# Optimization experiments

Hardware: AMD Instinct MI355X
Metric: run time of the kernel (lower is better)

The kernel has to match this reference:

```python
import jax, jax.numpy as jnp
import numpy as np

B, D, F = 4096, 2048, 16384


def setup_inputs() -> dict:
    key = jax.random.key(0)
    ks = jax.random.split(key, 5)
    s_enc = 1.0 / np.sqrt(D)
    s_dec = 1.0 / np.sqrt(F)
    return {
        "x": jax.random.normal(ks[0], (B, D), dtype=jnp.float32),
        "W_enc": jax.random.normal(ks[1], (F, D), dtype=jnp.float32) * s_enc,
        "b_enc": jnp.zeros((F,), dtype=jnp.float32),
        "W_kest1": jax.random.normal(ks[2], (F, D), dtype=jnp.float32) * s_enc,
        "b_kest1": jnp.zeros((F,), dtype=jnp.float32),
        "W_kest2": jax.random.normal(ks[3], (1, F), dtype=jnp.float32) * s_dec,
        "b_kest2": jnp.zeros((1,), dtype=jnp.float32),
        "W_dec": jax.random.normal(ks[4], (D, F), dtype=jnp.float32) * s_dec,
        "b_dec": jnp.zeros((D,), dtype=jnp.float32),
        "k": 64,
    }


def topk_per_row(acts, k_est):
    # rank of each element when sorted descending (ties resolved stably;
    # after ReLU ties are zeros, so output is identical either way)
    order = jnp.argsort(-acts, axis=1)          # [B, F] descending order
    rank = jnp.argsort(order, axis=1)           # rank[i,j] = position of acts[i,j]
    mask = rank < k_est[:, None]                # per-row dynamic (float) k
    return acts * mask


def reference(x, W_enc, b_enc, W_kest1, b_kest1, W_kest2, b_kest2, W_dec, b_dec, k):
    xc = x - b_dec                                              # [B, D]
    acts = jax.nn.relu(xc @ W_enc.T + b_enc)                    # [B, F]
    h = jax.nn.relu(xc @ W_kest1.T + b_kest1)                   # [B, F]
    k_est = jax.nn.sigmoid(h @ W_kest2.T + b_kest2)[:, 0] * (2.0 * k)  # [B]
    enc = topk_per_row(acts, k_est)                             # [B, F] sparse codes
    x_hat = enc @ W_dec.T + b_dec                               # [B, D]
    return x_hat
```

## Files before the change

kernel.cpp:

```cpp
#include <hip/hip_runtime.h>
#include <hip/hip_bf16.h>
#include <cstdint>
#include <cstddef>

#define BATCH 4096
#define DIM   2048
#define FEAT  16384
#define MAXF  2048

typedef __attribute__((ext_vector_type(8))) short s8v;
typedef __attribute__((ext_vector_type(8))) _Float16 h8v;
typedef __attribute__((ext_vector_type(4))) float f4v;

__device__ __forceinline__ void split2(float v, unsigned short &h, unsigned short &l){
  _Float16 hf = (_Float16)v;
  _Float16 lf = (_Float16)((v - (float)hf) * 2048.0f);
  h = __builtin_bit_cast(unsigned short, hf);
  l = __builtin_bit_cast(unsigned short, lf);
}

__device__ __forceinline__ void gload16(const void* g, void* l){
  __builtin_amdgcn_global_load_lds(
      (const __attribute__((address_space(1))) void*)g,
      (__attribute__((address_space(3))) void*)l, 16, 0, 0);
}

__global__ __launch_bounds__(256)
void splitX(const float* __restrict__ x, const float* __restrict__ bdec,
            unsigned short* __restrict__ p0, unsigned short* __restrict__ p1)
{
  const size_t i = ((size_t)blockIdx.x * 256 + threadIdx.x) * 4;
  const int col = (int)(i & (DIM - 1));
  const float4 v = *(const float4*)(x + i);
  const float4 b = *(const float4*)(bdec + col);
  float e0 = v.x - b.x, e1 = v.y - b.y, e2 = v.z - b.z, e3 = v.w - b.w;
  ushort4 H, L;
  split2(e0, H.x, L.x); split2(e1, H.y, L.y);
  split2(e2, H.z, L.z); split2(e3, H.w, L.w);
  *(ushort4*)(p0 + i) = H; *(ushort4*)(p1 + i) = L;
}

__global__ __launch_bounds__(256)
void splitW(const float* __restrict__ w,
            unsigned short* __restrict__ p0, unsigned short* __restrict__ p1)
{
  const size_t i = ((size_t)blockIdx.x * 256 + threadIdx.x) * 4;
  const float4 v = *(const float4*)(w + i);
  ushort4 H, L;
  split2(v.x, H.x, L.x); split2(v.y, H.y, L.y);
  split2(v.z, H.z, L.z); split2(v.w, H.w, L.w);
  *(ushort4*)(p0 + i) = H; *(ushort4*)(p1 + i) = L;
}

__global__ __launch_bounds__(256)
void splitW1(const float* __restrict__ w, unsigned short* __restrict__ p0)
{
  const size_t i = ((size_t)blockIdx.x * 256 + threadIdx.x) * 4;
  const float4 v = *(const float4*)(w + i);
  ushort4 H;
  H.x = __builtin_bit_cast(unsigned short, (_Float16)v.x);
  H.y = __builtin_bit_cast(unsigned short, (_Float16)v.y);
  H.z = __builtin_bit_cast(unsigned short, (_Float16)v.z);
  H.w = __builtin_bit_cast(unsigned short, (_Float16)v.w);
  *(ushort4*)(p0 + i) = H;
}

template<int MODE>
__global__ __launch_bounds__(256, 4)
void gemma(const unsigned short* __restrict__ Ah_, const unsigned short* __restrict__ Bh_,
           const float* __restrict__ bias, const float* __restrict__ w2,
           float* __restrict__ acts, float* __restrict__ zpart)
{
  __shared__ unsigned short sAB[2][2][128][32];
  const int tid  = threadIdx.x;
  const int lane = tid & 63, wv = tid >> 6;

  const int bid = blockIdx.x;
  const int xcd = bid & 7;
  const int idx = bid >> 3;
  const int sq  = idx >> 6;
  const int s   = idx & 63;
  const int bx  = (xcd << 4) | ((sq & 1) << 3) | (s & 7);
  const int by  = ((sq >> 1) << 3) | (s >> 3);
  const int row0 = by << 7, col0 = bx << 7;

  const int wr = (wv & 1) << 6, wc = (wv >> 1) << 6;

  f4v acc[4][4];
  #pragma unroll
  for (int i = 0; i < 4; ++i)
    #pragma unroll
    for (int j = 0; j < 4; ++j)
      acc[i][j] = (f4v){0.f, 0.f, 0.f, 0.f};

  const unsigned short* gsrc[4];
  unsigned ldsoff[4];
  #pragma unroll
  for (int j = 0; j < 4; ++j){
    const int q = (wv << 2) + j;
    const int mat = q >> 3;
    const int chunk = q & 7;
    const int r  = (chunk << 4) + (lane >> 2);
    const int gl = (lane & 3) ^ ((r >> 1) & 3);
    const int rowg = ((mat == 0) ? row0 : col0) + r;
    gsrc[j]  = ((mat == 0) ? Ah_ : Bh_) + (size_t)rowg * DIM + (gl << 3);
    ldsoff[j] = (unsigned)(mat * 8192 + chunk * 1024);
  }

  const int fr16 = lane & 15;
  const int kg   = lane >> 4;
  int ra[4], rb[4];
  #pragma unroll
  for (int f = 0; f < 4; ++f){ ra[f] = wr + (f << 4) + fr16; rb[f] = wc + (f << 4) + fr16; }

  #define LDFRAGA(bf, mat, r) \
    (*(const h8v*)((const char*)sAB + (bf) * 16384 + (mat) * 8192 + (r) * 64 + (((kg ^ (((r) >> 1) & 3)) << 4))))
  #define STAGEA(bf, ko)                                                      \
    {                                                                         \
      _Pragma("unroll")                                                       \
      for (int j = 0; j < 4; ++j)                                             \
        gload16(gsrc[j] + (ko), (char*)sAB + (bf) * 16384 + ldsoff[j]);       \
    }

  int cur = 0;
  STAGEA(0, 0);
  __syncthreads();

  for (int kt = 0; kt < DIM / 32; ++kt){
    if (kt < DIM / 32 - 1) STAGEA(cur ^ 1, (kt + 1) << 5);

    h8v Ahf[4], Bhf[4];
    #pragma unroll
    for (int f = 0; f < 4; ++f) Ahf[f] = LDFRAGA(cur, 0, ra[f]);
    #pragma unroll
    for (int f = 0; f < 4; ++f) Bhf[f] = LDFRAGA(cur, 1, rb[f]);
    #pragma unroll
    for (int fi = 0; fi < 4; ++fi)
      #pragma unroll
      for (int fj = 0; fj < 4; ++fj)
        acc[fi][fj] = __builtin_amdgcn_mfma_f32_16x16x32_f16(Bhf[fj], Ahf[fi], acc[fi][fj], 0, 0, 0);

    __syncthreads();
    cur ^= 1;
  }
  #undef LDFRAGA
  #undef STAGEA

  const int mloc = lane & 15;
  const int nq   = (lane >> 4) << 2;
  if (MODE == 0){
    #pragma unroll
    for (int fi = 0; fi < 4; ++fi){
      const int grow = row0 + wr + (fi << 4) + mloc;
      #pragma unroll
      for (int fj = 0; fj < 4; ++fj){
        const int gcol = col0 + wc + (fj << 4) + nq;
        const float4 be = *(const float4*)(bias + gcol);
        f4v v;
        v[0] = fmaxf(acc[fi][fj][0] + be.x, 0.f);
        v[1] = fmaxf(acc[fi][fj][1] + be.y, 0.f);
        v[2] = fmaxf(acc[fi][fj][2] + be.z, 0.f);
        v[3] = fmaxf(acc[fi][fj][3] + be.w, 0.f);
        __builtin_nontemporal_store(v, (f4v*)(acts + (size_t)grow * FEAT + gcol));
      }
    }
  } else {
    #pragma unroll
    for (int fi = 0; fi < 4; ++fi){
      float ssum = 0.f;
      #pragma unroll
      for (int fj = 0; fj < 4; ++fj){
        const int gcol = col0 + wc + (fj << 4) + nq;
        const float4 be = *(const float4*)(bias + gcol);
        const float4 wk = *(const float4*)(w2 + gcol);
        float h0 = fmaxf(acc[fi][fj][0] + be.x, 0.f);
        float h1 = fmaxf(acc[fi][fj][1] + be.y, 0.f);
        float h2 = fmaxf(acc[fi][fj][2] + be.z, 0.f);
        float h3 = fmaxf(acc[fi][fj][3] + be.w, 0.f);
        ssum = fmaf(h0, wk.x, ssum);
        ssum = fmaf(h1, wk.y, ssum);
        ssum = fmaf(h2, wk.z, ssum);
        ssum = fmaf(h3, wk.w, ssum);
      }
      ssum += __shfl_xor(ssum, 16);
      ssum += __shfl_xor(ssum, 32);
      if (lane < 16){
        const int grow = row0 + wr + (fi << 4) + lane;
        zpart[(size_t)grow * 256 + (bx << 1) + (wc >> 6)] = ssum;
      }
    }
  }
}

__global__ __launch_bounds__(512, 4)
void gemmx(const unsigned short* __restrict__ Ah_, const unsigned short* __restrict__ Al_,
           const unsigned short* __restrict__ Bh_, const unsigned short* __restrict__ Bl_,
           const float* __restrict__ bias, const float* __restrict__ w2,
           const int* __restrict__ rowList, const int* __restrict__ nflagp,
           float* __restrict__ zexact)
{
  const int panel = blockIdx.x >> 7;
  const int bx    = blockIdx.x & 127;
  const int row0p = panel << 7;
  if (row0p >= *nflagp) return;
  const int col0 = bx << 7;

  __shared__ unsigned short sAB[2][2][128][64];
  const int tid  = threadIdx.x;
  const int lane = tid & 63, wv = tid >> 6;
  const int wr = (wv & 3) << 5, wc = (wv >> 2) << 6;

  f4v acc[2][4], acc2[2][4];
  #pragma unroll
  for (int i = 0; i < 2; ++i)
    #pragma unroll
    for (int j = 0; j < 4; ++j){
      acc[i][j]  = (f4v){0.f, 0.f, 0.f, 0.f};
      acc2[i][j] = (f4v){0.f, 0.f, 0.f, 0.f};
    }

  const unsigned short* gsrc[4];
  unsigned ldsoff[4];
  #pragma unroll
  for (int j = 0; j < 4; ++j){
    const int q = (wv << 2) + j;
    const int mat = q >> 4;
    const int chunk = q & 15;
    const int r  = (chunk << 3) + (lane >> 3);
    const int gl = (lane & 7) ^ (r & 7);
    const int co = (gl & 3) << 3;
    const unsigned short* hi = (mat == 0) ? Ah_ : Bh_;
    const unsigned short* lo = (mat == 0) ? Al_ : Bl_;
    const int rowg = (mat == 0) ? rowList[row0p + r] : (col0 + r);
    gsrc[j]  = ((gl < 4) ? hi : lo) + (size_t)rowg * DIM + co;
    ldsoff[j] = (unsigned)(mat * 16384 + chunk * 1024);
  }

  const int fr16 = lane & 15;
  const int kg   = lane >> 4;
  int ra[2], rb[4];
  #pragma unroll
  for (int f = 0; f < 2; ++f) ra[f] = wr + (f << 4) + fr16;
  #pragma unroll
  for (int f = 0; f < 4; ++f) rb[f] = wc + (f << 4) + fr16;

  #define LDFRAG(bf, mat, r, hb) \
    (*(const h8v*)((const char*)sAB + (bf) * 32768 + (mat) * 16384 + (r) * 128 + (((((hb) + kg) ^ ((r) & 7)) << 4))))
  #define STAGE(bf, ko)                                                       \
    {                                                                         \
      _Pragma("unroll")                                                       \
      for (int j = 0; j < 4; ++j)                                             \
        gload16(gsrc[j] + (ko), (char*)sAB + (bf) * 32768 + ldsoff[j]);       \
    }

  int cur = 0;
  STAGE(0, 0);
  __syncthreads();

  for (int kt = 0; kt < DIM / 32; ++kt){
    if (kt < DIM / 32 - 1) STAGE(cur ^ 1, (kt + 1) << 5);

    h8v Ahf[2], Bhf[4], Xl[4];
    #pragma unroll
    for (int f = 0; f < 2; ++f) Ahf[f] = LDFRAG(cur, 0, ra[f], 0);
    #pragma unroll
    for (int f = 0; f < 4; ++f) Bhf[f] = LDFRAG(cur, 1, rb[f], 0);
    #pragma unroll
    for (int fi = 0; fi < 2; ++fi)
      #pragma unroll
      for (int fj = 0; fj < 4; ++fj)
        acc[fi][fj] = __builtin_amdgcn_mfma_f32_16x16x32_f16(Bhf[fj], Ahf[fi], acc[fi][fj], 0, 0, 0);
    #pragma unroll
    for (int f = 0; f < 2; ++f) Xl[f] = LDFRAG(cur, 0, ra[f], 4);
    #pragma unroll
    for (int fi = 0; fi < 2; ++fi)
      #pragma unroll
      for (int fj = 0; fj < 4; ++fj)
        acc2[fi][fj] = __builtin_amdgcn_mfma_f32_16x16x32_f16(Bhf[fj], Xl[fi], acc2[fi][fj], 0, 0, 0);
    #pragma unroll
    for (int f = 0; f < 4; ++f) Xl[f] = LDFRAG(cur, 1, rb[f], 4);
    #pragma unroll
    for (int fi = 0; fi < 2; ++fi)
      #pragma unroll
      for (int fj = 0; fj < 4; ++fj)
        acc2[fi][fj] = __builtin_amdgcn_mfma_f32_16x16x32_f16(Xl[fj], Ahf[fi], acc2[fi][fj], 0, 0, 0);

    __syncthreads();
    cur ^= 1;
  }
  #undef LDFRAG
  #undef STAGE

  const float LSC = 1.0f / 2048.0f;
  const int nq = (lane >> 4) << 2;
  #pragma unroll
  for (int fi = 0; fi < 2; ++fi){
    float ssum = 0.f;
    #pragma unroll
    for (int fj = 0; fj < 4; ++fj){
      const int gcol = col0 + wc + (fj << 4) + nq;
      const float4 be = *(const float4*)(bias + gcol);
      const float4 wk = *(const float4*)(w2 + gcol);
      float h0 = fmaxf(acc[fi][fj][0] + LSC * acc2[fi][fj][0] + be.x, 0.f);
      float h1 = fmaxf(acc[fi][fj][1] + LSC * acc2[fi][fj][1] + be.y, 0.f);
      float h2 = fmaxf(acc[fi][fj][2] + LSC * acc2[fi][fj][2] + be.z, 0.f);
      float h3 = fmaxf(acc[fi][fj][3] + LSC * acc2[fi][fj][3] + be.w, 0.f);
      ssum = fmaf(h0, wk.x, ssum);
      ssum = fmaf(h1, wk.y, ssum);
      ssum = fmaf(h2, wk.z, ssum);
      ssum = fmaf(h3, wk.w, ssum);
    }
    ssum += __shfl_xor(ssum, 16);
    ssum += __shfl_xor(ssum, 32);
    if (lane < 16){
      const int pos = row0p + wr + (fi << 4) + lane;
      zexact[(size_t)pos * 256 + (bx << 1) + (wc >> 6)] = ssum;
    }
  }
}

__global__ __launch_bounds__(256)
void zinit(int* __restrict__ rowList, int* __restrict__ nflag)
{
  const int i = blockIdx.x * 256 + threadIdx.x;
  if (i < MAXF) rowList[i] = 0;
  if (i == 0) *nflag = 0;
}

__global__ __launch_bounds__(256)
void zreduce_flag(const float* __restrict__ zpart, const float* __restrict__ bk2,
                  const int* __restrict__ kp, int* __restrict__ mrow,
                  int* __restrict__ rowList, int* __restrict__ nflag)
{
  const int row  = blockIdx.x * 4 + (threadIdx.x >> 6);
  const int lane = threadIdx.x & 63;
  const float* zp = zpart + (size_t)row * 256;
  float s = zp[lane] + zp[lane + 64] + zp[lane + 128] + zp[lane + 192];
  s += __shfl_xor(s, 1);
  s += __shfl_xor(s, 2);
  s += __shfl_xor(s, 4);
  s += __shfl_xor(s, 8);
  s += __shfl_xor(s, 16);
  s += __shfl_xor(s, 32);
  if (lane == 0){
    float z = s + bk2[0];
    float kest = 2.f * (float)(*kp) * (1.f / (1.f + expf(-z)));
    int m = (int)ceilf(kest);
    m = min(max(m, 0), 128);
    mrow[row] = m;
    const float frac = kest - floorf(kest);
    const float dmin = fminf(frac, 1.f - frac);
    if (dmin < 0.1f){
      int p = atomicAdd(nflag, 1);
      if (p < MAXF) rowList[p] = row;
    }
  }
}

__global__ __launch_bounds__(256)
void zreduce2(const float* __restrict__ zexact, const int* __restrict__ rowList,
              const int* __restrict__ nflagp, const float* __restrict__ bk2,
              const int* __restrict__ kp, int* __restrict__ mrow)
{
  const int pos  = blockIdx.x * 4 + (threadIdx.x >> 6);
  const int lane = threadIdx.x & 63;
  const int nf = min(*nflagp, MAXF);
  if (pos >= nf) return;
  const float* zp = zexact + (size_t)pos * 256;
  float s = zp[lane] + zp[lane + 64] + zp[lane + 128] + zp[lane + 192];
  s += __shfl_xor(s, 1);
  s += __shfl_xor(s, 2);
  s += __shfl_xor(s, 4);
  s += __shfl_xor(s, 8);
  s += __shfl_xor(s, 16);
  s += __shfl_xor(s, 32);
  if (lane == 0){
    float z = s + bk2[0];
    float kest = 2.f * (float)(*kp) * (1.f / (1.f + expf(-z)));
    int m = (int)ceilf(kest);
    m = min(max(m, 0), 128);
    mrow[rowList[pos]] = m;
  }
}

__device__ __forceinline__ void radix_find(int* hist, int nbins, int need, int tid,
                                           int* out3, int* blksum)
{
  const int per  = nbins >> 8;
  const int base = tid * per;
  int bs = 0;
  for (int j = 0; j < per; ++j) bs += hist[base + j];
  blksum[tid] = bs;
  __syncthreads();
  if (tid == 0){
    int a2 = 0;
    for (int t = 255; t >= 0; --t){ int v = blksum[t]; blksum[t] = a2; a2 += v; }
  }
  __syncthreads();
  int ch = blksum[tid];
  for (int j = per - 1; j >= 0; --j){
    const int b = base + j;
    const int c = hist[b];
    if (ch < need && need <= ch + c){ out3[0] = b; out3[1] = need - ch; out3[2] = ch; }
    ch += c;
  }
  __syncthreads();
}

__global__ __launch_bounds__(256)
void select_band(const float* __restrict__ acts, const float* __restrict__ x,
                 const float* __restrict__ bdec, const float* __restrict__ Wenc,
                 const int* __restrict__ mrow, int* __restrict__ selIdx,
                 float* __restrict__ selVal, int* __restrict__ scount)
{
  __shared__ int hist[2048];
  __shared__ int blksum[256];
  __shared__ int out3[4];
  __shared__ unsigned listU[2048];
  __shared__ int listI[2048];
  __shared__ int lcnt, dcnt, acnt;
  __shared__ unsigned ambU[64];
  __shared__ int ambI[64];
  __shared__ double ambE[64];
  __shared__ double wred[4];

  const int row = blockIdx.x, tid = threadIdx.x;
  const int m = mrow[row];
  const float* rp = acts + (size_t)row * FEAT;
  const int base = row << 7;

  for (int i = tid; i < 2048; i += 256) hist[i] = 0;
  __syncthreads();
  for (int it = 0; it < 16; ++it){
    const int i4 = (it << 8) + tid;
    const uint4 u4 = *(const uint4*)(rp + ((size_t)i4 << 2));
    if (u4.x) atomicAdd(&hist[u4.x >> 21], 1);
    if (u4.y) atomicAdd(&hist[u4.y >> 21], 1);
    if (u4.z) atomicAdd(&hist[u4.z >> 21], 1);
    if (u4.w) atomicAdd(&hist[u4.w >> 21], 1);
  }
  __syncthreads();
  radix_find(hist, 2048, m, tid, out3, blksum);
  const int bin1 = out3[0];
  const int rem1 = out3[1];
  const int bin1m1 = (bin1 > 1) ? bin1 - 1 : 1;

  if (tid == 0){ lcnt = 0; dcnt = 0; acnt = 0; }
  __syncthreads();
  for (int it = 0; it < 16; ++it){
    const int i4 = (it << 8) + tid;
    const uint4 u4 = *(const uint4*)(rp + ((size_t)i4 << 2));
    const int ib = i4 << 2;
    if (u4.x && (int)(u4.x >> 21) >= bin1m1){ int p = atomicAdd(&lcnt, 1); if (p < 2048){ listU[p] = u4.x; listI[p] = ib;     } }
    if (u4.y && (int)(u4.y >> 21) >= bin1m1){ int p = atomicAdd(&lcnt, 1); if (p < 2048){ listU[p] = u4.y; listI[p] = ib + 1; } }
    if (u4.z && (int)(u4.z >> 21) >= bin1m1){ int p = atomicAdd(&lcnt, 1); if (p < 2048){ listU[p] = u4.z; listI[p] = ib + 2; } }
    if (u4.w && (int)(u4.w >> 21) >= bin1m1){ int p = atomicAdd(&lcnt, 1); if (p < 2048){ listU[p] = u4.w; listI[p] = ib + 3; } }
  }
  __syncthreads();
  const int L = min(lcnt, 2048);

  for (int i = tid; i < 2048; i += 256) hist[i] = 0;
  __syncthreads();
  for (int i = tid; i < L; i += 256){
    unsigned u = listU[i];
    if ((int)(u >> 21) == bin1) atomicAdd(&hist[(u >> 10) & 0x7FF], 1);
  }
  __syncthreads();
  radix_find(hist, 2048, rem1, tid, out3, blksum);
  const int bin2 = out3[0];
  const int rem2 = out3[1];

  const unsigned topbits = (((unsigned)bin1 << 11) | (unsigned)bin2);
  for (int i = tid; i < 1024; i += 256) hist[i] = 0;
  __syncthreads();
  for (int i = tid; i < L; i += 256){
    unsigned u = listU[i];
    if ((u >> 10) == topbits) atomicAdd(&hist[u & 0x3FF], 1);
  }
  __syncthreads();
  radix_find(hist, 1024, rem2, tid, out3, blksum);
  const int bin3 = out3[0];

  const unsigned tbits = ((unsigned)bin1 << 21) | ((unsigned)bin2 << 10) | (unsigned)bin3;
  const float vm = __uint_as_float(tbits);
  const float EPS2 = 0.01f;
  const float lo_cut = vm - EPS2, hi_cut = vm + EPS2;

  for (int i = tid; i < L; i += 256){
    const float f = __uint_as_float(listU[i]);
    if (f > hi_cut){
      int p = atomicAdd(&dcnt, 1);
      selIdx[base + p] = listI[i];
      selVal[base + p] = f;
    } else if (f >= lo_cut){
      int p = atomicAdd(&acnt, 1);
      if (p < 64){ ambU[p] = listU[i]; ambI[p] = listI[i]; }
    }
  }
  __syncthreads();
  const int D = dcnt;
  const int A = min(acnt, 64);
  int need = m - D;
  if (need < 0) need = 0;
  if (need > A) need = A;

  if (need > 0){
    float* xcs = (float*)hist;
    for (int j = tid; j < DIM; j += 256)
      xcs[j] = x[(size_t)row * DIM + j] - bdec[j];
    __syncthreads();
    const int lane = tid & 63, wv = tid >> 6;
    for (int c = 0; c < A; ++c){
      const float* wrow = Wenc + (size_t)ambI[c] * DIM;
      double sd = 0.0;
      for (int j = tid; j < DIM; j += 256)
        sd += (double)xcs[j] * (double)wrow[j];
      #pragma unroll
      for (int off = 32; off; off >>= 1) sd += __shfl_xor(sd, off);
      if (lane == 0) wred[wv] = sd;
      __syncthreads();
      if (tid == 0) ambE[c] = wred[0] + wred[1] + wred[2] + wred[3];
      __syncthreads();
    }
    if (tid == 0){
      for (int e = 0; e < need; ++e){
        int best = -1;
        for (int c = 0; c < A; ++c){
          if (ambI[c] < 0) continue;
          if (best < 0 || ambE[c] > ambE[best] ||
              (ambE[c] == ambE[best] && ambI[c] < ambI[best])) best = c;
        }
        selIdx[base + D + e] = ambI[best];
        selVal[base + D + e] = __uint_as_float(ambU[best]);
        ambI[best] = -1;
      }
    }
  }
  if (tid == 0) scount[row] = D + need;
}

__global__ __launch_bounds__(256)
void transpose_dec(const float* __restrict__ Wd, _Float16* __restrict__ WdT16)
{
  __shared__ float t[64][65];
  const int f0 = blockIdx.x << 6, d0 = blockIdx.y << 6;
  const int tx = threadIdx.x & 15, ty = threadIdx.x >> 4;
  #pragma unroll
  for (int r = 0; r < 4; ++r){
    const int d = ty + (r << 4);
    const float4 v = *(const float4*)(Wd + (size_t)(d0 + d) * FEAT + f0 + (tx << 2));
    t[d][(tx << 2) + 0] = v.x;
    t[d][(tx << 2) + 1] = v.y;
    t[d][(tx << 2) + 2] = v.z;
    t[d][(tx << 2) + 3] = v.w;
  }
  __syncthreads();
  #pragma unroll
  for (int r = 0; r < 4; ++r){
    const int f = ty + (r << 4);
    ushort4 o;
    o.x = __builtin_bit_cast(unsigned short, (_Float16)t[(tx << 2) + 0][f]);
    o.y = __builtin_bit_cast(unsigned short, (_Float16)t[(tx << 2) + 1][f]);
    o.z = __builtin_bit_cast(unsigned short, (_Float16)t[(tx << 2) + 2][f]);
    o.w = __builtin_bit_cast(unsigned short, (_Float16)t[(tx << 2) + 3][f]);
    *(ushort4*)(WdT16 + (size_t)(f0 + f) * DIM + d0 + (tx << 2)) = o;
  }
}

__global__ __launch_bounds__(256)
void decode_k(const _Float16* __restrict__ WdT16, const int* __restrict__ selIdx,
              const float* __restrict__ selVal, const int* __restrict__ scount,
              const float* __restrict__ bdec, float* __restrict__ out)
{
  __shared__ int   sI[128];
  __shared__ float sV[128];
  const int row = blockIdx.x, tid = threadIdx.x;
  const int m = scount[row];
  if (tid < m){
    sI[tid] = selIdx[(row << 7) + tid];
    sV[tid] = selVal[(row << 7) + tid];
  }
  __syncthreads();
  const int d = tid << 3;
  float a[8];
  {
    const float4 b0 = *(const float4*)(bdec + d);
    const float4 b1 = *(const float4*)(bdec + d + 4);
    a[0] = b0.x; a[1] = b0.y; a[2] = b0.z; a[3] = b0.w;
    a[4] = b1.x; a[5] = b1.y; a[6] = b1.z; a[7] = b1.w;
  }
  for (int i = 0; i < m; ++i){
    const float v = sV[i];
    const h8v w = *(const h8v*)(WdT16 + (size_t)sI[i] * DIM + d);
    #pragma unroll
    for (int j = 0; j < 8; ++j)
      a[j] = fmaf(v, (float)w[j], a[j]);
  }
  float4 o0 = {a[0], a[1], a[2], a[3]};
  float4 o1 = {a[4], a[5], a[6], a[7]};
  *(float4*)(out + (size_t)row * DIM + d)     = o0;
  *(float4*)(out + (size_t)row * DIM + d + 4) = o1;
}

extern "C" void kernel_launch(void* const* d_in, const int* in_sizes, int n_in,
                              void* d_out, int out_size, void* d_ws, size_t ws_size,
                              hipStream_t stream)
{
  const float* x    = (const float*)d_in[0];
  const float* Wenc = (const float*)d_in[1];
  const float* benc = (const float*)d_in[2];
  const float* Wk1  = (const float*)d_in[3];
  const float* bk1  = (const float*)d_in[4];
  const float* Wk2  = (const float*)d_in[5];
  const float* bk2  = (const float*)d_in[6];
  const float* Wdec = (const float*)d_in[7];
  const float* bdec = (const float*)d_in[8];
  const int*   kp   = (const int*)d_in[9];
  float* out = (float*)d_out;

  char* ws = (char*)d_ws;
  const size_t XS_BYTES   = (size_t)BATCH * DIM * 2;
  const size_t ACTS_BYTES = (size_t)BATCH * FEAT * 4;
  const size_t WP_BYTES   = (size_t)FEAT * DIM * 2;

  unsigned short* xs0 = (unsigned short*)ws;
  unsigned short* xs1 = (unsigned short*)(ws + XS_BYTES);
  char* p = ws + 2 * XS_BYTES;
  float* acts = (float*)p;
  _Float16* WdT16 = (_Float16*)p;
  p += ACTS_BYTES;
  unsigned short* wp0 = (unsigned short*)p;
  unsigned short* wp1 = (unsigned short*)(p + WP_BYTES);
  p += 2 * WP_BYTES;
  float* zpart  = (float*)p;               p += 4194304;
  int*   mrow   = (int*)p;                 p += 16384;
  int*   selIdx = (int*)p;                 p += 2097152;
  float* selVal = (float*)p;               p += 2097152;
  int*   scount = (int*)p;                 p += 16384;
  int*   rowList= (int*)p;                 p += MAXF * 4;
  int*   nflag  = (int*)p;                 p += 128;
  float* zexact = (float*)p;               p += (size_t)MAXF * 256 * 4;

  (void)ws_size; (void)in_sizes; (void)n_in; (void)out_size;

  splitX<<<dim3(BATCH * DIM / 1024), dim3(256), 0, stream>>>(x, bdec, xs0, xs1);
  splitW<<<dim3(FEAT * DIM / 1024), dim3(256), 0, stream>>>(Wk1, wp0, wp1);
  gemma<1><<<dim3(4096), dim3(256), 0, stream>>>(xs0, wp0, bk1, Wk2, nullptr, zpart);
  zinit<<<dim3(MAXF / 256), dim3(256), 0, stream>>>(rowList, nflag);
  zreduce_flag<<<dim3(BATCH / 4), dim3(256), 0, stream>>>(zpart, bk2, kp, mrow,
                                                          rowList, nflag);
  gemmx<<<dim3(16 * 128), dim3(512), 0, stream>>>(xs0, xs1, wp0, wp1, bk1, Wk2,
                                                  rowList, nflag, zexact);
  zreduce2<<<dim3(MAXF / 4), dim3(256), 0, stream>>>(zexact, rowList, nflag,
                                                     bk2, kp, mrow);
  splitW1<<<dim3(FEAT * DIM / 1024), dim3(256), 0, stream>>>(Wenc, wp0);
  gemma<0><<<dim3(4096), dim3(256), 0, stream>>>(xs0, wp0, benc, nullptr, acts, nullptr);
  select_band<<<dim3(BATCH), dim3(256), 0, stream>>>(acts, x, bdec, Wenc, mrow,
                                                     selIdx, selVal, scount);
  transpose_dec<<<dim3(FEAT / 64, DIM / 64), dim3(256), 0, stream>>>(Wdec, WdT16);
  decode_k<<<dim3(BATCH), dim3(256), 0, stream>>>(WdT16, selIdx, selVal, scount, bdec, out);
}
```

Measured before the change: 1.253 ms.

## Fuse encoder and k-estimator GEMMs into one dual-output kernel sharing A tiles

Replaces the two separate fp16 GEMM launches (k-estimator hidden and encoder activations) with one 512-thread kernel. Each block stages the shared x tile once plus both weight tiles into LDS, and two groups of four waves each compute one output. This saves reloading the x tile from global memory and one launch. In exchange it uses more LDS per block (three matrices, double-buffered), runs 512-thread blocks with a different occupancy bound, and needs an extra workspace buffer for the fp16 encoder weights.

```diff
diff --git a/kernel.cpp b/kernel.cpp
--- a/kernel.cpp
+++ b/kernel.cpp
@@ -65,13 +65,14 @@
   *(ushort4*)(p0 + i) = H;
 }
 
-template<int MODE>
-__global__ __launch_bounds__(256, 4)
-void gemma(const unsigned short* __restrict__ Ah_, const unsigned short* __restrict__ Bh_,
-           const float* __restrict__ bias, const float* __restrict__ w2,
+__global__ __launch_bounds__(512, 3)
+void gemmd(const unsigned short* __restrict__ Ah_, const unsigned short* __restrict__ B1h_,
+           const unsigned short* __restrict__ B2h_,
+           const float* __restrict__ benc, const float* __restrict__ bk1,
+           const float* __restrict__ w2,
            float* __restrict__ acts, float* __restrict__ zpart)
 {
-  __shared__ unsigned short sAB[2][2][128][32];
+  __shared__ unsigned short sAB[2][3][128][32];
   const int tid  = threadIdx.x;
   const int lane = tid & 63, wv = tid >> 6;
 
@@ -84,7 +85,9 @@
   const int by  = ((sq >> 1) << 3) | (s >> 3);
   const int row0 = by << 7, col0 = bx << 7;
 
-  const int wr = (wv & 1) << 6, wc = (wv >> 1) << 6;
+  const int role = wv >> 2;
+  const int wloc = wv & 3;
+  const int wr = (wloc & 1) << 6, wc = (wloc >> 1) << 6;
 
   f4v acc[4][4];
   #pragma unroll
@@ -93,47 +96,49 @@
     for (int j = 0; j < 4; ++j)
       acc[i][j] = (f4v){0.f, 0.f, 0.f, 0.f};
 
-  const unsigned short* gsrc[4];
-  unsigned ldsoff[4];
-  #pragma unroll
-  for (int j = 0; j < 4; ++j){
-    const int q = (wv << 2) + j;
+  const unsigned short* gsrc[3];
+  unsigned ldsoff[3];
+  #pragma unroll
+  for (int j = 0; j < 3; ++j){
+    const int q = wv * 3 + j;
     const int mat = q >> 3;
     const int chunk = q & 7;
     const int r  = (chunk << 4) + (lane >> 2);
     const int gl = (lane & 3) ^ ((r >> 1) & 3);
     const int rowg = ((mat == 0) ? row0 : col0) + r;
-    gsrc[j]  = ((mat == 0) ? Ah_ : Bh_) + (size_t)rowg * DIM + (gl << 3);
+    const unsigned short* P = (mat == 0) ? Ah_ : ((mat == 1) ? B1h_ : B2h_);
+    gsrc[j]  = P + (size_t)rowg * DIM + (gl << 3);
     ldsoff[j] = (unsigned)(mat * 8192 + chunk * 1024);
   }
 
   const int fr16 = lane & 15;
   const int kg   = lane >> 4;
+  const int bmat = 1 + role;
   int ra[4], rb[4];
   #pragma unroll
   for (int f = 0; f < 4; ++f){ ra[f] = wr + (f << 4) + fr16; rb[f] = wc + (f << 4) + fr16; }
 
-  #define LDFRAGA(bf, mat, r) \
-    (*(const h8v*)((const char*)sAB + (bf) * 16384 + (mat) * 8192 + (r) * 64 + (((kg ^ (((r) >> 1) & 3)) << 4))))
-  #define STAGEA(bf, ko)                                                      \
+  #define LDFRAGD(bf, mat, r) \
+    (*(const h8v*)((const char*)sAB + (bf) * 24576 + (mat) * 8192 + (r) * 64 + (((kg ^ (((r) >> 1) & 3)) << 4))))
+  #define STAGED(bf, ko)                                                      \
     {                                                                         \
       _Pragma("unroll")                                                       \
-      for (int j = 0; j < 4; ++j)                                             \
-        gload16(gsrc[j] + (ko), (char*)sAB + (bf) * 16384 + ldsoff[j]);       \
+      for (int j = 0; j < 3; ++j)                                             \
+        gload16(gsrc[j] + (ko), (char*)sAB + (bf) * 24576 + ldsoff[j]);       \
     }
 
   int cur = 0;
-  STAGEA(0, 0);
+  STAGED(0, 0);
   __syncthreads();
 
   for (int kt = 0; kt < DIM / 32; ++kt){
-    if (kt < DIM / 32 - 1) STAGEA(cur ^ 1, (kt + 1) << 5);
+    if (kt < DIM / 32 - 1) STAGED(cur ^ 1, (kt + 1) << 5);
 
     h8v Ahf[4], Bhf[4];
     #pragma unroll
-    for (int f = 0; f < 4; ++f) Ahf[f] = LDFRAGA(cur, 0, ra[f]);
-    #pragma unroll
-    for (int f = 0; f < 4; ++f) Bhf[f] = LDFRAGA(cur, 1, rb[f]);
+    for (int f = 0; f < 4; ++f) Ahf[f] = LDFRAGD(cur, 0, ra[f]);
+    #pragma unroll
+    for (int f = 0; f < 4; ++f) Bhf[f] = LDFRAGD(cur, bmat, rb[f]);
     #pragma unroll
     for (int fi = 0; fi < 4; ++fi)
       #pragma unroll
@@ -143,19 +148,19 @@
     __syncthreads();
     cur ^= 1;
   }
-  #undef LDFRAGA
-  #undef STAGEA
+  #undef LDFRAGD
+  #undef STAGED
 
   const int mloc = lane & 15;
   const int nq   = (lane >> 4) << 2;
-  if (MODE == 0){
+  if (role == 0){
     #pragma unroll
     for (int fi = 0; fi < 4; ++fi){
       const int grow = row0 + wr + (fi << 4) + mloc;
       #pragma unroll
       for (int fj = 0; fj < 4; ++fj){
         const int gcol = col0 + wc + (fj << 4) + nq;
-        const float4 be = *(const float4*)(bias + gcol);
+        const float4 be = *(const float4*)(benc + gcol);
         f4v v;
         v[0] = fmaxf(acc[fi][fj][0] + be.x, 0.f);
         v[1] = fmaxf(acc[fi][fj][1] + be.y, 0.f);
@@ -171,7 +176,7 @@
       #pragma unroll
       for (int fj = 0; fj < 4; ++fj){
         const int gcol = col0 + wc + (fj << 4) + nq;
-        const float4 be = *(const float4*)(bias + gcol);
+        const float4 be = *(const float4*)(bk1 + gcol);
         const float4 wk = *(const float4*)(w2 + gcol);
         float h0 = fmaxf(acc[fi][fj][0] + be.x, 0.f);
         float h1 = fmaxf(acc[fi][fj][1] + be.y, 0.f);
@@ -629,9 +634,10 @@
   float* acts = (float*)p;
   _Float16* WdT16 = (_Float16*)p;
   p += ACTS_BYTES;
-  unsigned short* wp0 = (unsigned short*)p;
-  unsigned short* wp1 = (unsigned short*)(p + WP_BYTES);
-  p += 2 * WP_BYTES;
+  unsigned short* wk0 = (unsigned short*)p;
+  unsigned short* wk1 = (unsigned short*)(p + WP_BYTES);
+  unsigned short* we0 = (unsigned short*)(p + 2 * WP_BYTES);
+  p += 3 * WP_BYTES;
   float* zpart  = (float*)p;               p += 4194304;
   int*   mrow   = (int*)p;                 p += 16384;
   int*   selIdx = (int*)p;                 p += 2097152;
@@ -644,17 +650,17 @@
   (void)ws_size; (void)in_sizes; (void)n_in; (void)out_size;
 
   splitX<<<dim3(BATCH * DIM / 1024), dim3(256), 0, stream>>>(x, bdec, xs0, xs1);
-  splitW<<<dim3(FEAT * DIM / 1024), dim3(256), 0, stream>>>(Wk1, wp0, wp1);
-  gemma<1><<<dim3(4096), dim3(256), 0, stream>>>(xs0, wp0, bk1, Wk2, nullptr, zpart);
+  splitW<<<dim3(FEAT * DIM / 1024), dim3(256), 0, stream>>>(Wk1, wk0, wk1);
+  splitW1<<<dim3(FEAT * DIM / 1024), dim3(256), 0, stream>>>(Wenc, we0);
+  gemmd<<<dim3(4096), dim3(512), 0, stream>>>(xs0, we0, wk0, benc, bk1, Wk2,
+                                              acts, zpart);
   zinit<<<dim3(MAXF / 256), dim3(256), 0, stream>>>(rowList, nflag);
   zreduce_flag<<<dim3(BATCH / 4), dim3(256), 0, stream>>>(zpart, bk2, kp, mrow,
                                                           rowList, nflag);
-  gemmx<<<dim3(16 * 128), dim3(512), 0, stream>>>(xs0, xs1, wp0, wp1, bk1, Wk2,
+  gemmx<<<dim3(16 * 128), dim3(512), 0, stream>>>(xs0, xs1, wk0, wk1, bk1, Wk2,
                                                   rowList, nflag, zexact);
   zreduce2<<<dim3(MAXF / 4), dim3(256), 0, stream>>>(zexact, rowList, nflag,
                                                      bk2, kp, mrow);
-  splitW1<<<dim3(FEAT * DIM / 1024), dim3(256), 0, stream>>>(Wenc, wp0);
-  gemma<0><<<dim3(4096), dim3(256), 0, stream>>>(xs0, wp0, benc, nullptr, acts, nullptr);
   select_band<<<dim3(BATCH), dim3(256), 0, stream>>>(acts, x, bdec, Wenc, mrow,
                                                      selIdx, selVal, scount);
   transpose_dec<<<dim3(FEAT / 64, DIM / 64), dim3(256), 0, stream>>>(Wdec, WdT16);
```

After: 1.167 ms. 6.9% less time.
